# Kernel optimization log

Measured on AMD Instinct MI355X. Metric: run time of the kernel, lower is better.

## Reference

```python
import jax, jax.numpy as jnp
import numpy as np
import math

BH, N_Q, D = 32, 1024, 128
N_K_PREFIX = 8192
TOPK = 64


def setup_inputs() -> dict:
    key = jax.random.key(0)
    k1, k2, k3, k4, k5 = jax.random.split(key, 5)
    return {
        "query_states": jax.random.normal(k1, (BH, N_Q, D), dtype=jnp.float32),
        "suffix_key_states": jax.random.normal(k2, (BH, N_Q, D), dtype=jnp.float32),
        "suffix_value_states": jax.random.normal(k3, (BH, N_Q, D), dtype=jnp.float32),
        "prefix_key_states": jax.random.normal(k4, (BH, N_K_PREFIX, D), dtype=jnp.float32),
        "prefix_value_states": jax.random.normal(k5, (BH, N_K_PREFIX, D), dtype=jnp.float32),
        "topk_k": TOPK,
    }


def reference(query_states, suffix_key_states, suffix_value_states,
              prefix_key_states, prefix_value_states, topk_k):
    BH_, N_q, D_ = query_states.shape
    scale = 1.0 / math.sqrt(D_)

    # --- exact FAISS inner-product search over prefix keys, per (batch,head) ---
    # scores_prefix: (BH, N_q, N_k_prefix)
    scores_prefix = jnp.einsum("bnd,bkd->bnk", query_states, prefix_key_states) * scale
    topk_values, topk_indices = jax.lax.top_k(scores_prefix, topk_k)  # (BH, N_q, k)

    # exp of sparse (prefix) scores; original code uses raw exp (no max-subtract)
    topk_values_exp = jnp.exp(topk_values)                    # (BH, N_q, k)
    topk_values_exp_sums = topk_values_exp.sum(axis=-1)       # (BH, N_q)

    # --- dense causal attention over suffix ---
    score_dense = jnp.einsum("bnd,bkd->bnk", query_states, suffix_key_states) * scale
    if N_q > 1:
        causal = jnp.triu(jnp.ones((N_q, N_q), dtype=bool), k=1)
        score_dense = jnp.where(causal[None], -jnp.inf, score_dense)
    score_dense_exp = jnp.exp(score_dense)                    # (BH, N_q, N_q)
    score_dense_exp_sums = score_dense_exp.sum(axis=-1)       # (BH, N_q)

    # --- joint softmax denominator over prefix top-k + dense suffix ---
    denom = topk_values_exp_sums + score_dense_exp_sums       # (BH, N_q)
    attn_dense = score_dense_exp / denom[:, :, None]
    attn_sparse = topk_values_exp / denom[:, :, None]

    # gather top-k prefix values: (BH, N_q, k, D)
    gathered_v = jnp.take_along_axis(
        prefix_value_states[:, None, :, :], topk_indices[:, :, :, None], axis=2
    )

    out = jnp.einsum("bnk,bkd->bnd", attn_dense, suffix_value_states)
    out = out + jnp.einsum("bnk,bnkd->bnd", attn_sparse, gathered_v)
    return out
```

## Files before the change

### kernel.cpp

```cpp
#include <hip/hip_runtime.h>
#include <math.h>

#define BH 32
#define NQ 1024
#define DDIM 128
#define NK 8192
#define TOPK 64
#define QTP 128
#define CAP 224
#define NPL 28
#define CSTRIDE 225
#define NSEL 80
#define NSL 10
#define KEY_SENT 0x7FFFFFFF
#define SCALE 0.08838834764831845f

using short8 = __attribute__((ext_vector_type(8))) short;
using f32x4  = __attribute__((ext_vector_type(4))) float;

__device__ __forceinline__ float dot4acc(float acc, float4 a, float4 b) {
  acc = fmaf(a.x, b.x, acc);
  acc = fmaf(a.y, b.y, acc);
  acc = fmaf(a.z, b.z, acc);
  acc = fmaf(a.w, b.w, acc);
  return acc;
}

__device__ __forceinline__ short8 cvt8hi(float4 v0, float4 v1) {
  float f[8] = {v0.x, v0.y, v0.z, v0.w, v1.x, v1.y, v1.z, v1.w};
  short8 h;
  #pragma unroll
  for (int i = 0; i < 8; ++i) {
    unsigned int uu = __float_as_uint(f[i]);
    h[i] = (short)((uu + 0x7FFFu + ((uu >> 16) & 1u)) >> 16);
  }
  return h;
}

__device__ __forceinline__ void cvt8(float4 v0, float4 v1, short8& hi, short8& lo) {
  float f[8] = {v0.x, v0.y, v0.z, v0.w, v1.x, v1.y, v1.z, v1.w};
  #pragma unroll
  for (int i = 0; i < 8; ++i) {
    unsigned int uu = __float_as_uint(f[i]);
    unsigned int hb = (uu + 0x7FFFu + ((uu >> 16) & 1u)) >> 16;
    float rem = f[i] - __uint_as_float(hb << 16);
    unsigned int ul = __float_as_uint(rem);
    unsigned int lb = (ul + 0x7FFFu + ((ul >> 16) & 1u)) >> 16;
    hi[i] = (short)hb;
    lo[i] = (short)lb;
  }
}

__device__ __forceinline__ unsigned short bf16_split(float f, float& rem) {
  unsigned int u = __float_as_uint(f);
  unsigned int hb = (u + 0x7FFFu + ((u >> 16) & 1u)) >> 16;
  rem = f - __uint_as_float(hb << 16);
  return (unsigned short)hb;
}

__global__ __launch_bounds__(512, 2) void prefix_kernel(
    const float* __restrict__ Q, const float* __restrict__ PK,
    const float* __restrict__ PV, float* __restrict__ out,
    float* __restrict__ sums)
{
  __shared__ short khi[128][136];
  __shared__ unsigned int cpk[QTP][CSTRIDE];
  __shared__ int ccnt[QTP];
  __shared__ float thr[QTP];

  const int bid = (int)blockIdx.x;
  const int xcd = bid & 7;
  const int sl  = bid >> 3;
  const int qt  = sl & 7;
  const int b   = xcd + ((sl >> 3) << 3);
  const int q0 = qt * QTP;
  const int tid = (int)threadIdx.x;
  const int lane = tid & 63;
  const int wid = tid >> 6;
  const int lrow = lane & 15;
  const int lko  = (lane >> 4) << 3;
  const int rbase = (wid & 1) << 6;
  const int kbase = (wid >> 1) << 5;

  const float* Qb = Q + ((size_t)b * NQ + q0) * DDIM;
  const float* Kb = PK + (size_t)b * NK * DDIM;

  if (tid < QTP) {
    ccnt[tid] = 0;
    const float* qp = Qb + (size_t)tid * DDIM;
    float s = 0.f;
    for (int d = 0; d < DDIM; d += 4) {
      float4 v = *(const float4*)(qp + d);
      s = fmaf(v.x, v.x, fmaf(v.y, v.y, fmaf(v.z, v.z, fmaf(v.w, v.w, s))));
    }
    thr[tid] = 2.1f * sqrtf(s) * SCALE;
  }

  short8 ahi[4][4];
  #pragma unroll
  for (int rt = 0; rt < 4; ++rt) {
    const float* qrow = Qb + (size_t)(rbase + rt * 16 + lrow) * DDIM;
    #pragma unroll
    for (int t = 0; t < 4; ++t) {
      float4 f0 = *(const float4*)(qrow + t * 32 + lko);
      float4 f1 = *(const float4*)(qrow + t * 32 + lko + 4);
      ahi[rt][t] = cvt8hi(f0, f1);
    }
  }
  __syncthreads();

  float thr8[4][4];
  #pragma unroll
  for (int rt = 0; rt < 4; ++rt)
    #pragma unroll
    for (int j = 0; j < 4; ++j)
      thr8[rt][j] = thr[rbase + rt * 16 + ((lane >> 4) << 2) + j];

  const int srow0 = tid >> 4;
  const int sc8  = (tid & 15) << 3;
  float4 cur[4][2];
  #pragma unroll
  for (int p = 0; p < 4; ++p) {
    const float* src = Kb + (size_t)(srow0 + (p << 5)) * DDIM + sc8;
    cur[p][0] = *(const float4*)src;
    cur[p][1] = *(const float4*)(src + 4);
  }

  const f32x4 vzero = {0.f, 0.f, 0.f, 0.f};

  for (int k0 = 0; k0 < NK; k0 += 128) {
    #pragma unroll
    for (int p = 0; p < 4; ++p)
      *(short8*)&khi[srow0 + (p << 5)][sc8] = cvt8hi(cur[p][0], cur[p][1]);
    __syncthreads();
    if (k0 + 128 < NK) {
      #pragma unroll
      for (int p = 0; p < 4; ++p) {
        const float* src = Kb + (size_t)(k0 + 128 + srow0 + (p << 5)) * DDIM + sc8;
        cur[p][0] = *(const float4*)src;
        cur[p][1] = *(const float4*)(src + 4);
      }
    }
    f32x4 acc[4][2];
    #pragma unroll
    for (int rt = 0; rt < 4; ++rt)
      #pragma unroll
      for (int kt = 0; kt < 2; ++kt)
        acc[rt][kt] = vzero;
    #pragma unroll
    for (int t = 0; t < 4; ++t) {
      #pragma unroll
      for (int kt = 0; kt < 2; ++kt) {
        const int krow = kbase + kt * 16 + lrow;
        short8 bhi = *(const short8*)&khi[krow][t * 32 + lko];
        #pragma unroll
        for (int rt = 0; rt < 4; ++rt)
          acc[rt][kt] = __builtin_amdgcn_mfma_f32_16x16x32_bf16(ahi[rt][t], bhi, acc[rt][kt], 0, 0, 0);
      }
    }
    #pragma unroll
    for (int rt = 0; rt < 4; ++rt) {
      #pragma unroll
      for (int kt = 0; kt < 2; ++kt) {
        const int key = k0 + kbase + kt * 16 + lrow;
        #pragma unroll
        for (int j = 0; j < 4; ++j) {
          float s = acc[rt][kt][j] * SCALE;
          if (s > thr8[rt][j]) {
            const int grow = rbase + rt * 16 + ((lane >> 4) << 2) + j;
            int slot = atomicAdd(&ccnt[grow], 1);
            if (slot < CAP) {
              unsigned int us = __float_as_uint(s);
              unsigned int bf = (us + 0x7FFFu + ((us >> 16) & 1u)) >> 16;
              cpk[grow][slot] = (bf << 13) | (unsigned int)(8191 - key);
            }
          }
        }
      }
    }
    __syncthreads();
  }

  const int lane8 = tid & 7;
  const float* Vb = PV + (size_t)b * NK * DDIM;

  for (int pass = 0; pass < 2; ++pass) {
    const int rr = (tid >> 3) + (pass << 6);
    const int cn = min(ccnt[rr], CAP);

    unsigned int myc[NPL];
    #pragma unroll
    for (int k = 0; k < NPL; ++k) {
      const int c = lane8 + (k << 3);
      myc[k] = (c < cn) ? cpk[rr][c] : 0u;
    }

    int selkey[NSL];
    #pragma unroll
    for (int j = 0; j < NSL; ++j) selkey[j] = KEY_SENT;
    unsigned int mask = 0;
    #pragma unroll
    for (int t = 0; t < NSEL; ++t) {
      unsigned int bvp = 0u; int bk = -1;
      #pragma unroll
      for (int k = 0; k < NPL; ++k) {
        if (!((mask >> k) & 1u) && myc[k] > bvp) { bvp = myc[k]; bk = k; }
      }
      const unsigned int pv = bvp;
      #pragma unroll
      for (int m = 4; m >= 1; m >>= 1) {
        unsigned int ov = (unsigned int)__shfl_xor((int)bvp, m, 8);
        if (ov > bvp) bvp = ov;
      }
      if (bk >= 0 && pv == bvp) mask |= (1u << bk);
      if ((t & 7) == lane8)
        selkey[t >> 3] = (bvp == 0u) ? KEY_SENT : (8191 - (int)(bvp & 0x1FFFu));
    }

    const float* Qrow = Qb + (size_t)rr * DDIM;
    float mys[NSL];
    #pragma unroll
    for (int j = 0; j < NSL; ++j) {
      const int key = selkey[j];
      float s = -1e30f;
      if (key < NK) {
        const float* kp = Kb + (size_t)key * DDIM;
        float a = 0.f;
        for (int c4 = 0; c4 < 32; ++c4) {
          float4 qv = *(const float4*)(Qrow + (c4 << 2));
          float4 kv = *(const float4*)(kp + (c4 << 2));
          a = dot4acc(a, qv, kv);
        }
        s = a * SCALE;
      }
      mys[j] = s;
    }

    {
      unsigned int mask2 = 0;
      float esum = 0.f;
      f32x4 g0 = {0.f, 0.f, 0.f, 0.f};
      f32x4 g1 = {0.f, 0.f, 0.f, 0.f};
      f32x4 g2 = {0.f, 0.f, 0.f, 0.f};
      f32x4 g3 = {0.f, 0.f, 0.f, 0.f};
      for (int t = 0; t < TOPK; ++t) {
        float bv = -1e30f; int bkey = KEY_SENT; int bj = -1;
        #pragma unroll
        for (int j = 0; j < NSL; ++j) {
          if (!((mask2 >> j) & 1u)) {
            if (mys[j] > bv || (mys[j] == bv && selkey[j] < bkey)) {
              bv = mys[j]; bkey = selkey[j]; bj = j;
            }
          }
        }
        const float pv = bv; const int pk = bkey;
        #pragma unroll
        for (int m = 4; m >= 1; m >>= 1) {
          float ov = __shfl_xor(bv, m, 8);
          int okey = __shfl_xor(bkey, m, 8);
          if (ov > bv || (ov == bv && okey < bkey)) { bv = ov; bkey = okey; }
        }
        if (bj >= 0 && pv == bv && pk == bkey) mask2 |= (1u << bj);
        if (bkey < NK) {
          const float e = expf(bv);
          esum += e;
          const float* vp = Vb + (size_t)bkey * DDIM + (lane8 << 4);
          g0 += e * *(const f32x4*)(vp);
          g1 += e * *(const f32x4*)(vp + 4);
          g2 += e * *(const f32x4*)(vp + 8);
          g3 += e * *(const f32x4*)(vp + 12);
        }
      }
      if (lane8 == 0) sums[(size_t)b * NQ + q0 + rr] = esum;
      float* op = out + ((size_t)b * NQ + q0 + rr) * DDIM + (lane8 << 4);
      *(f32x4*)(op)      = g0;
      *(f32x4*)(op + 4)  = g1;
      *(f32x4*)(op + 8)  = g2;
      *(f32x4*)(op + 12) = g3;
    }
  }
}

__global__ __launch_bounds__(512, 2) void dense_mfma_kernel(
    const float* __restrict__ Q, const float* __restrict__ SK,
    const float* __restrict__ SV, float* __restrict__ out,
    const float* __restrict__ sums)
{
  __shared__ short khi[64][136];
  __shared__ short klo[64][136];
  __shared__ short vthi[128][72];
  __shared__ short vtlo[128][72];
  __shared__ short phi_l[64][72];
  __shared__ short plo_l[64][72];
  __shared__ float dsum[64];

  const int bid = (int)blockIdx.x;
  const int p  = bid >> 5;
  const int b  = bid & 31;
  const int tid = (int)threadIdx.x;
  const int lane = tid & 63;
  const int wid = tid >> 6;
  const int lrow = lane & 15;
  const int lk8  = (lane >> 4) << 3;
  const int rt   = wid & 3;
  const int half = wid >> 2;
  const int rbase = rt << 4;
  const int crow  = (lane >> 4) << 2;

  const float* Qb = Q + (size_t)b * NQ * DDIM;
  const float* Kb = SK + (size_t)b * NQ * DDIM;
  const float* Vb = SV + (size_t)b * NQ * DDIM;

  const int skey = tid >> 3;
  const int sd16 = (tid & 7) << 4;

  const f32x4 vzero = {0.f, 0.f, 0.f, 0.f};

  for (int ht = 0; ht < 2; ++ht) {
    const int tno = (ht == 0) ? p : (15 - p);
    const int q0t = tno * 64;
    const int kend = q0t + 64;

    if (tid < 64) dsum[tid] = 0.f;

    short8 ahi[4], alo[4];
    {
      const float* qrow = Qb + (size_t)(q0t + rbase + lrow) * DDIM;
      #pragma unroll
      for (int t = 0; t < 4; ++t) {
        float4 f0 = *(const float4*)(qrow + t * 32 + lk8);
        float4 f1 = *(const float4*)(qrow + t * 32 + lk8 + 4);
        cvt8(f0, f1, ahi[t], alo[t]);
      }
    }

    f32x4 accv[4];
    #pragma unroll
    for (int dt = 0; dt < 4; ++dt) accv[dt] = vzero;
    float es[4] = {0.f, 0.f, 0.f, 0.f};

    __syncthreads();

    for (int c0 = 0; c0 < kend; c0 += 64) {
      {
        const float* src = Kb + (size_t)(c0 + skey) * DDIM + sd16;
        float4 a0 = *(const float4*)src;
        float4 a1 = *(const float4*)(src + 4);
        float4 a2 = *(const float4*)(src + 8);
        float4 a3 = *(const float4*)(src + 12);
        short8 h, l;
        cvt8(a0, a1, h, l);
        *(short8*)&khi[skey][sd16] = h;
        *(short8*)&klo[skey][sd16] = l;
        cvt8(a2, a3, h, l);
        *(short8*)&khi[skey][sd16 + 8] = h;
        *(short8*)&klo[skey][sd16 + 8] = l;
      }
      {
        const float* src = Vb + (size_t)(c0 + skey) * DDIM + sd16;
        #pragma unroll
        for (int i4 = 0; i4 < 4; ++i4) {
          f32x4 v = *(const f32x4*)(src + i4 * 4);
          #pragma unroll
          for (int jj = 0; jj < 4; ++jj) {
            float rem, rem2;
            unsigned short h = bf16_split(v[jj], rem);
            unsigned short l = bf16_split(rem, rem2);
            vthi[sd16 + i4 * 4 + jj][skey] = (short)h;
            vtlo[sd16 + i4 * 4 + jj][skey] = (short)l;
          }
        }
      }
      __syncthreads();

      f32x4 aq[2];
      aq[0] = vzero; aq[1] = vzero;
      #pragma unroll
      for (int t = 0; t < 4; ++t) {
        #pragma unroll
        for (int kt2 = 0; kt2 < 2; ++kt2) {
          const int krow = half * 32 + kt2 * 16 + lrow;
          short8 bhi = *(const short8*)&khi[krow][t * 32 + lk8];
          short8 blo = *(const short8*)&klo[krow][t * 32 + lk8];
          aq[kt2] = __builtin_amdgcn_mfma_f32_16x16x32_bf16(ahi[t], bhi, aq[kt2], 0, 0, 0);
          aq[kt2] = __builtin_amdgcn_mfma_f32_16x16x32_bf16(alo[t], bhi, aq[kt2], 0, 0, 0);
          aq[kt2] = __builtin_amdgcn_mfma_f32_16x16x32_bf16(ahi[t], blo, aq[kt2], 0, 0, 0);
        }
      }

      #pragma unroll
      for (int kt2 = 0; kt2 < 2; ++kt2) {
        const int keyl = half * 32 + kt2 * 16 + lrow;
        const int key_g = c0 + keyl;
        #pragma unroll
        for (int j = 0; j < 4; ++j) {
          const int row_l = rbase + crow + j;
          const int row_g = q0t + row_l;
          const float s = aq[kt2][j] * SCALE;
          const float e = (key_g <= row_g) ? expf(s) : 0.f;
          es[j] += e;
          float rem, rem2;
          unsigned short h = bf16_split(e, rem);
          unsigned short l = bf16_split(rem, rem2);
          phi_l[row_l][keyl] = (short)h;
          plo_l[row_l][keyl] = (short)l;
        }
      }
      __syncthreads();

      #pragma unroll
      for (int t2 = 0; t2 < 2; ++t2) {
        short8 pah = *(const short8*)&phi_l[rbase + lrow][t2 * 32 + lk8];
        short8 pal = *(const short8*)&plo_l[rbase + lrow][t2 * 32 + lk8];
        #pragma unroll
        for (int dt = 0; dt < 4; ++dt) {
          const int ncol = half * 64 + dt * 16 + lrow;
          short8 bh = *(const short8*)&vthi[ncol][t2 * 32 + lk8];
          short8 bl = *(const short8*)&vtlo[ncol][t2 * 32 + lk8];
          accv[dt] = __builtin_amdgcn_mfma_f32_16x16x32_bf16(pah, bh, accv[dt], 0, 0, 0);
          accv[dt] = __builtin_amdgcn_mfma_f32_16x16x32_bf16(pal, bh, accv[dt], 0, 0, 0);
          accv[dt] = __builtin_amdgcn_mfma_f32_16x16x32_bf16(pah, bl, accv[dt], 0, 0, 0);
        }
      }
      __syncthreads();
    }

    #pragma unroll
    for (int m = 8; m >= 1; m >>= 1) {
      #pragma unroll
      for (int j = 0; j < 4; ++j) es[j] += __shfl_xor(es[j], m, 16);
    }
    if (lrow == 0) {
      #pragma unroll
      for (int j = 0; j < 4; ++j)
        atomicAdd(&dsum[rbase + crow + j], es[j]);
    }
    __syncthreads();

    #pragma unroll
    for (int j = 0; j < 4; ++j) {
      const int row_l = rbase + crow + j;
      const float denom = dsum[row_l] + sums[(size_t)b * NQ + q0t + row_l];
      const float inv = 1.0f / denom;
      float* orow = out + ((size_t)b * NQ + q0t + row_l) * DDIM;
      #pragma unroll
      for (int dt = 0; dt < 4; ++dt) {
        const int d = half * 64 + dt * 16 + lrow;
        orow[d] = (orow[d] + accv[dt][j]) * inv;
      }
    }
    __syncthreads();
  }
}

extern "C" void kernel_launch(void* const* d_in, const int* in_sizes, int n_in,
                              void* d_out, int out_size, void* d_ws, size_t ws_size,
                              hipStream_t stream) {
  const float* Q  = (const float*)d_in[0];
  const float* SK = (const float*)d_in[1];
  const float* SV = (const float*)d_in[2];
  const float* PK = (const float*)d_in[3];
  const float* PV = (const float*)d_in[4];
  float* out = (float*)d_out;
  float* sums = (float*)d_ws;

  prefix_kernel<<<dim3(BH * 8), dim3(512), 0, stream>>>(Q, PK, PV, out, sums);
  dense_mfma_kernel<<<dim3(256), dim3(512), 0, stream>>>(Q, SK, SV, out, sums);
}
```

Measured before the change: 788.1 us.

## Split prefix top-k into a key-sliced screen kernel and a per-row select kernel

The fused prefix kernel is replaced by two kernels. A screen kernel holds all 1024 queries of a head in one block and scans one 1024-key slice, so each prefix key tile is loaded and converted to bf16 once per head rather than once per query tile. It writes above-threshold key indices to a global candidate list using atomics. A select kernel then rescans every candidate (up to 224 per row) with exact fp32 dot products and drops the old bf16 pre-selection of 80. This adds a memset, an extra launch and many more exact K gathers. Candidates that overflow the cap are kept in atomic arrival order rather than by score.

```diff
diff --git a/kernel.cpp b/kernel.cpp
--- a/kernel.cpp
+++ b/kernel.cpp
@@ -6,14 +6,14 @@
 #define DDIM 128
 #define NK 8192
 #define TOPK 64
-#define QTP 128
 #define CAP 224
 #define NPL 28
-#define CSTRIDE 225
-#define NSEL 80
-#define NSL 10
+#define SCAP 48
 #define KEY_SENT 0x7FFFFFFF
 #define SCALE 0.08838834764831845f
+
+#define WS_GCNT_OFF 131072
+#define WS_GKEY_OFF 262144
 
 using short8 = __attribute__((ext_vector_type(8))) short;
 using f32x4  = __attribute__((ext_vector_type(4))) float;
@@ -58,34 +58,29 @@
   return (unsigned short)hb;
 }
 
-__global__ __launch_bounds__(512, 2) void prefix_kernel(
+__global__ __launch_bounds__(1024, 4) void screen_kernel(
     const float* __restrict__ Q, const float* __restrict__ PK,
-    const float* __restrict__ PV, float* __restrict__ out,
-    float* __restrict__ sums)
+    unsigned short* __restrict__ gkeys, int* __restrict__ gcnt)
 {
   __shared__ short khi[128][136];
-  __shared__ unsigned int cpk[QTP][CSTRIDE];
-  __shared__ int ccnt[QTP];
-  __shared__ float thr[QTP];
+  __shared__ unsigned short cand[1024][SCAP];
+  __shared__ int ccnt[1024];
+  __shared__ float thr[1024];
 
   const int bid = (int)blockIdx.x;
-  const int xcd = bid & 7;
-  const int sl  = bid >> 3;
-  const int qt  = sl & 7;
-  const int b   = xcd + ((sl >> 3) << 3);
-  const int q0 = qt * QTP;
+  const int b = bid & 31;
+  const int slice = bid >> 5;
   const int tid = (int)threadIdx.x;
   const int lane = tid & 63;
   const int wid = tid >> 6;
   const int lrow = lane & 15;
   const int lko  = (lane >> 4) << 3;
-  const int rbase = (wid & 1) << 6;
-  const int kbase = (wid >> 1) << 5;
-
-  const float* Qb = Q + ((size_t)b * NQ + q0) * DDIM;
+  const int rbase = wid << 6;
+
+  const float* Qb = Q + (size_t)b * NQ * DDIM;
   const float* Kb = PK + (size_t)b * NK * DDIM;
 
-  if (tid < QTP) {
+  {
     ccnt[tid] = 0;
     const float* qp = Qb + (size_t)tid * DDIM;
     float s = 0.f;
@@ -116,168 +111,155 @@
     for (int j = 0; j < 4; ++j)
       thr8[rt][j] = thr[rbase + rt * 16 + ((lane >> 4) << 2) + j];
 
-  const int srow0 = tid >> 4;
-  const int sc8  = (tid & 15) << 3;
-  float4 cur[4][2];
-  #pragma unroll
-  for (int p = 0; p < 4; ++p) {
-    const float* src = Kb + (size_t)(srow0 + (p << 5)) * DDIM + sc8;
-    cur[p][0] = *(const float4*)src;
-    cur[p][1] = *(const float4*)(src + 4);
-  }
-
   const f32x4 vzero = {0.f, 0.f, 0.f, 0.f};
-
-  for (int k0 = 0; k0 < NK; k0 += 128) {
-    #pragma unroll
-    for (int p = 0; p < 4; ++p)
-      *(short8*)&khi[srow0 + (p << 5)][sc8] = cvt8hi(cur[p][0], cur[p][1]);
+  const int srow = tid >> 3;
+  const int sc16 = (tid & 7) << 4;
+
+  for (int c = 0; c < 8; ++c) {
+    const int k0c = (slice << 10) + (c << 7);
     __syncthreads();
-    if (k0 + 128 < NK) {
-      #pragma unroll
-      for (int p = 0; p < 4; ++p) {
-        const float* src = Kb + (size_t)(k0 + 128 + srow0 + (p << 5)) * DDIM + sc8;
-        cur[p][0] = *(const float4*)src;
-        cur[p][1] = *(const float4*)(src + 4);
-      }
-    }
-    f32x4 acc[4][2];
-    #pragma unroll
-    for (int rt = 0; rt < 4; ++rt)
-      #pragma unroll
-      for (int kt = 0; kt < 2; ++kt)
-        acc[rt][kt] = vzero;
-    #pragma unroll
-    for (int t = 0; t < 4; ++t) {
-      #pragma unroll
-      for (int kt = 0; kt < 2; ++kt) {
-        const int krow = kbase + kt * 16 + lrow;
-        short8 bhi = *(const short8*)&khi[krow][t * 32 + lko];
+    {
+      const float* src = Kb + (size_t)(k0c + srow) * DDIM + sc16;
+      float4 v0 = *(const float4*)src;
+      float4 v1 = *(const float4*)(src + 4);
+      float4 v2 = *(const float4*)(src + 8);
+      float4 v3 = *(const float4*)(src + 12);
+      *(short8*)&khi[srow][sc16] = cvt8hi(v0, v1);
+      *(short8*)&khi[srow][sc16 + 8] = cvt8hi(v2, v3);
+    }
+    __syncthreads();
+
+    for (int kt = 0; kt < 8; ++kt) {
+      f32x4 acc[4];
+      #pragma unroll
+      for (int rt = 0; rt < 4; ++rt) acc[rt] = vzero;
+      #pragma unroll
+      for (int t = 0; t < 4; ++t) {
+        short8 bhi = *(const short8*)&khi[kt * 16 + lrow][t * 32 + lko];
         #pragma unroll
         for (int rt = 0; rt < 4; ++rt)
-          acc[rt][kt] = __builtin_amdgcn_mfma_f32_16x16x32_bf16(ahi[rt][t], bhi, acc[rt][kt], 0, 0, 0);
-      }
-    }
-    #pragma unroll
-    for (int rt = 0; rt < 4; ++rt) {
-      #pragma unroll
-      for (int kt = 0; kt < 2; ++kt) {
-        const int key = k0 + kbase + kt * 16 + lrow;
+          acc[rt] = __builtin_amdgcn_mfma_f32_16x16x32_bf16(ahi[rt][t], bhi, acc[rt], 0, 0, 0);
+      }
+      const int key = k0c + kt * 16 + lrow;
+      #pragma unroll
+      for (int rt = 0; rt < 4; ++rt) {
+        const int growb = rbase + rt * 16 + ((lane >> 4) << 2);
         #pragma unroll
         for (int j = 0; j < 4; ++j) {
-          float s = acc[rt][kt][j] * SCALE;
+          float s = acc[rt][j] * SCALE;
           if (s > thr8[rt][j]) {
-            const int grow = rbase + rt * 16 + ((lane >> 4) << 2) + j;
-            int slot = atomicAdd(&ccnt[grow], 1);
-            if (slot < CAP) {
-              unsigned int us = __float_as_uint(s);
-              unsigned int bf = (us + 0x7FFFu + ((us >> 16) & 1u)) >> 16;
-              cpk[grow][slot] = (bf << 13) | (unsigned int)(8191 - key);
-            }
+            const int row = growb + j;
+            int slot = atomicAdd(&ccnt[row], 1);
+            if (slot < SCAP) cand[row][slot] = (unsigned short)key;
           }
         }
       }
     }
-    __syncthreads();
-  }
-
+  }
+  __syncthreads();
+
+  {
+    const int r = tid;
+    const int n = min(ccnt[r], SCAP);
+    const int gr = b * NQ + r;
+    if (n > 0) {
+      int base = atomicAdd(&gcnt[gr], n);
+      for (int i = 0; i < n; ++i) {
+        const int dst = base + i;
+        if (dst < CAP) gkeys[(size_t)gr * CAP + dst] = cand[r][i];
+      }
+    }
+  }
+}
+
+__global__ __launch_bounds__(512, 2) void select_kernel(
+    const float* __restrict__ Q, const float* __restrict__ PK,
+    const float* __restrict__ PV, const unsigned short* __restrict__ gkeys,
+    const int* __restrict__ gcnt, float* __restrict__ out,
+    float* __restrict__ sums)
+{
+  const int bid = (int)blockIdx.x;
+  const int xcd = bid & 7;
+  const int sl  = bid >> 3;
+  const int tile = sl & 15;
+  const int b   = xcd + ((sl >> 4) << 3);
+  const int q0  = tile * 64;
+  const int tid = (int)threadIdx.x;
   const int lane8 = tid & 7;
+  const int rr = q0 + (tid >> 3);
+  const int gr = b * NQ + rr;
+
+  const float* Kb = PK + (size_t)b * NK * DDIM;
   const float* Vb = PV + (size_t)b * NK * DDIM;
 
-  for (int pass = 0; pass < 2; ++pass) {
-    const int rr = (tid >> 3) + (pass << 6);
-    const int cn = min(ccnt[rr], CAP);
-
-    unsigned int myc[NPL];
-    #pragma unroll
-    for (int k = 0; k < NPL; ++k) {
-      const int c = lane8 + (k << 3);
-      myc[k] = (c < cn) ? cpk[rr][c] : 0u;
-    }
-
-    int selkey[NSL];
-    #pragma unroll
-    for (int j = 0; j < NSL; ++j) selkey[j] = KEY_SENT;
-    unsigned int mask = 0;
-    #pragma unroll
-    for (int t = 0; t < NSEL; ++t) {
-      unsigned int bvp = 0u; int bk = -1;
-      #pragma unroll
-      for (int k = 0; k < NPL; ++k) {
-        if (!((mask >> k) & 1u) && myc[k] > bvp) { bvp = myc[k]; bk = k; }
-      }
-      const unsigned int pv = bvp;
+  const int cn = min(gcnt[gr], CAP);
+  int myi[NPL];
+  #pragma unroll
+  for (int k = 0; k < NPL; ++k) {
+    const int c = lane8 + (k << 3);
+    myi[k] = (c < cn) ? (int)gkeys[(size_t)gr * CAP + c] : KEY_SENT;
+  }
+
+  const float* Qrow = Q + (size_t)gr * DDIM;
+  float mys[NPL];
+  #pragma unroll
+  for (int j = 0; j < NPL; ++j) {
+    const int key = myi[j];
+    float s = -1e30f;
+    if (key < NK) {
+      const float* kp = Kb + (size_t)key * DDIM;
+      float a = 0.f;
+      for (int c4 = 0; c4 < 32; ++c4) {
+        float4 qv = *(const float4*)(Qrow + (c4 << 2));
+        float4 kv = *(const float4*)(kp + (c4 << 2));
+        a = dot4acc(a, qv, kv);
+      }
+      s = a * SCALE;
+    }
+    mys[j] = s;
+  }
+
+  {
+    unsigned int mask2 = 0;
+    float esum = 0.f;
+    f32x4 g0 = {0.f, 0.f, 0.f, 0.f};
+    f32x4 g1 = {0.f, 0.f, 0.f, 0.f};
+    f32x4 g2 = {0.f, 0.f, 0.f, 0.f};
+    f32x4 g3 = {0.f, 0.f, 0.f, 0.f};
+    for (int t = 0; t < TOPK; ++t) {
+      float bv = -1e30f; int bkey = KEY_SENT; int bj = -1;
+      #pragma unroll
+      for (int j = 0; j < NPL; ++j) {
+        if (!((mask2 >> j) & 1u)) {
+          if (mys[j] > bv || (mys[j] == bv && myi[j] < bkey)) {
+            bv = mys[j]; bkey = myi[j]; bj = j;
+          }
+        }
+      }
+      const float pv = bv; const int pk = bkey;
       #pragma unroll
       for (int m = 4; m >= 1; m >>= 1) {
-        unsigned int ov = (unsigned int)__shfl_xor((int)bvp, m, 8);
-        if (ov > bvp) bvp = ov;
-      }
-      if (bk >= 0 && pv == bvp) mask |= (1u << bk);
-      if ((t & 7) == lane8)
-        selkey[t >> 3] = (bvp == 0u) ? KEY_SENT : (8191 - (int)(bvp & 0x1FFFu));
-    }
-
-    const float* Qrow = Qb + (size_t)rr * DDIM;
-    float mys[NSL];
-    #pragma unroll
-    for (int j = 0; j < NSL; ++j) {
-      const int key = selkey[j];
-      float s = -1e30f;
-      if (key < NK) {
-        const float* kp = Kb + (size_t)key * DDIM;
-        float a = 0.f;
-        for (int c4 = 0; c4 < 32; ++c4) {
-          float4 qv = *(const float4*)(Qrow + (c4 << 2));
-          float4 kv = *(const float4*)(kp + (c4 << 2));
-          a = dot4acc(a, qv, kv);
-        }
-        s = a * SCALE;
-      }
-      mys[j] = s;
-    }
-
-    {
-      unsigned int mask2 = 0;
-      float esum = 0.f;
-      f32x4 g0 = {0.f, 0.f, 0.f, 0.f};
-      f32x4 g1 = {0.f, 0.f, 0.f, 0.f};
-      f32x4 g2 = {0.f, 0.f, 0.f, 0.f};
-      f32x4 g3 = {0.f, 0.f, 0.f, 0.f};
-      for (int t = 0; t < TOPK; ++t) {
-        float bv = -1e30f; int bkey = KEY_SENT; int bj = -1;
-        #pragma unroll
-        for (int j = 0; j < NSL; ++j) {
-          if (!((mask2 >> j) & 1u)) {
-            if (mys[j] > bv || (mys[j] == bv && selkey[j] < bkey)) {
-              bv = mys[j]; bkey = selkey[j]; bj = j;
-            }
-          }
-        }
-        const float pv = bv; const int pk = bkey;
-        #pragma unroll
-        for (int m = 4; m >= 1; m >>= 1) {
-          float ov = __shfl_xor(bv, m, 8);
-          int okey = __shfl_xor(bkey, m, 8);
-          if (ov > bv || (ov == bv && okey < bkey)) { bv = ov; bkey = okey; }
-        }
-        if (bj >= 0 && pv == bv && pk == bkey) mask2 |= (1u << bj);
-        if (bkey < NK) {
-          const float e = expf(bv);
-          esum += e;
-          const float* vp = Vb + (size_t)bkey * DDIM + (lane8 << 4);
-          g0 += e * *(const f32x4*)(vp);
-          g1 += e * *(const f32x4*)(vp + 4);
-          g2 += e * *(const f32x4*)(vp + 8);
-          g3 += e * *(const f32x4*)(vp + 12);
-        }
-      }
-      if (lane8 == 0) sums[(size_t)b * NQ + q0 + rr] = esum;
-      float* op = out + ((size_t)b * NQ + q0 + rr) * DDIM + (lane8 << 4);
-      *(f32x4*)(op)      = g0;
-      *(f32x4*)(op + 4)  = g1;
-      *(f32x4*)(op + 8)  = g2;
-      *(f32x4*)(op + 12) = g3;
-    }
+        float ov = __shfl_xor(bv, m, 8);
+        int okey = __shfl_xor(bkey, m, 8);
+        if (ov > bv || (ov == bv && okey < bkey)) { bv = ov; bkey = okey; }
+      }
+      if (bj >= 0 && pv == bv && pk == bkey) mask2 |= (1u << bj);
+      if (bkey < NK) {
+        const float e = expf(bv);
+        esum += e;
+        const float* vp = Vb + (size_t)bkey * DDIM + (lane8 << 4);
+        g0 += e * *(const f32x4*)(vp);
+        g1 += e * *(const f32x4*)(vp + 4);
+        g2 += e * *(const f32x4*)(vp + 8);
+        g3 += e * *(const f32x4*)(vp + 12);
+      }
+    }
+    if (lane8 == 0) sums[gr] = esum;
+    float* op = out + (size_t)gr * DDIM + (lane8 << 4);
+    *(f32x4*)(op)      = g0;
+    *(f32x4*)(op + 4)  = g1;
+    *(f32x4*)(op + 8)  = g2;
+    *(f32x4*)(op + 12) = g3;
   }
 }
 
@@ -464,6 +446,11 @@
   float* out = (float*)d_out;
   float* sums = (float*)d_ws;
 
-  prefix_kernel<<<dim3(BH * 8), dim3(512), 0, stream>>>(Q, PK, PV, out, sums);
+  int* gcnt = (int*)((char*)d_ws + WS_GCNT_OFF);
+  unsigned short* gkeys = (unsigned short*)((char*)d_ws + WS_GKEY_OFF);
+
+  hipMemsetAsync(gcnt, 0, (size_t)BH * NQ * sizeof(int), stream);
+  screen_kernel<<<dim3(256), dim3(1024), 0, stream>>>(Q, PK, gkeys, gcnt);
+  select_kernel<<<dim3(512), dim3(512), 0, stream>>>(Q, PK, PV, gkeys, gcnt, out, sums);
   dense_mfma_kernel<<<dim3(256), dim3(512), 0, stream>>>(Q, SK, SV, out, sums);
 }
```

New measurement: 941.2 us. 19.4% more time.
